# Optimization experiments

Hardware: AMD Instinct MI355X
Metric: run time of the kernel (lower is better)

## Reference

```python
import jax, jax.numpy as jnp
import numpy as np

N_NODES = 50000


def gcn_conv(x, W, b, src, dst, n_nodes):
    """PyG-style GCNConv: add self-loops, symmetric norm, transform-then-aggregate."""
    E = src.shape[0]
    loop = jnp.arange(n_nodes, dtype=src.dtype)
    src_sl = jnp.concatenate([src, loop])  # [E + N]
    dst_sl = jnp.concatenate([dst, loop])
    # degree (incl. self loops) at destination nodes, unit edge weights
    deg = jax.ops.segment_sum(jnp.ones(E + n_nodes, dtype=x.dtype), dst_sl,
                              num_segments=n_nodes)
    deg_inv_sqrt = jnp.where(deg > 0, jax.lax.rsqrt(deg), 0.0)
    norm = deg_inv_sqrt[src_sl] * deg_inv_sqrt[dst_sl]  # [E + N]
    h = x @ W  # [N, out] transform first (cheaper than transforming messages)
    msg = h[src_sl] * norm[:, None]  # gather + scale, [E+N, out]
    out = jax.ops.segment_sum(msg, dst_sl, num_segments=n_nodes)  # scatter-add
    return out + b


def setup_inputs() -> dict:
    key = jax.random.key(0)
    k = jax.random.split(key, 8)
    in_f, hid = 128, 128
    E, EL = 800000, 200000
    x = jax.random.normal(k[0], (N_NODES, in_f), dtype=jnp.float32)
    edge_index = jax.random.randint(k[1], (2, E), 0, N_NODES, dtype=jnp.int64)
    edge_label_index = jax.random.randint(k[2], (2, EL), 0, N_NODES, dtype=jnp.int64)
    s1 = 1.0 / np.sqrt(in_f)
    s2 = 1.0 / np.sqrt(hid)
    W1 = jax.random.uniform(k[3], (in_f, hid), jnp.float32, -s1, s1)
    b1 = jnp.zeros((hid,), jnp.float32)
    W2 = jax.random.uniform(k[4], (hid, hid), jnp.float32, -s2, s2)
    b2 = jnp.zeros((hid,), jnp.float32)
    return {"x": x, "edge_index": edge_index, "edge_label_index": edge_label_index,
            "W1": W1, "b1": b1, "W2": W2, "b2": b2}


def reference(x, edge_index, edge_label_index, W1, b1, W2, b2):
    src, dst = edge_index[0], edge_index[1]
    z = gcn_conv(x, W1, b1, src, dst, N_NODES)
    z = jax.nn.relu(z)
    z = gcn_conv(z, W2, b2, src, dst, N_NODES)
    ls, ld = edge_label_index[0], edge_label_index[1]
    prob = jnp.sum(z[ls] * z[ld], axis=1)  # gather-dot decode, [E_label]
    return jax.nn.sigmoid(prob)
```

## Files before the change

### kernel.cpp

```cpp
#include <hip/hip_runtime.h>
#include <hip/hip_fp16.h>
#include <math.h>

#define NN 50000
#define F 128
#define NB 512

typedef _Float16 half8 __attribute__((ext_vector_type(8)));
typedef float floatx4 __attribute__((ext_vector_type(4)));
typedef unsigned int uintx4 __attribute__((ext_vector_type(4)));

__global__ __launch_bounds__(256) void hist_kernel(const int* __restrict__ dst,
                                                   int* __restrict__ blockhist, int E) {
    __shared__ int h[256];
    int t = threadIdx.x;
    h[t] = 0;
    __syncthreads();
    int chunk = (E + NB - 1) / NB;
    int s = blockIdx.x * chunk;
    int e = min(E, s + chunk);
    for (int i = s + t; i < e; i += 256) atomicAdd(&h[dst[i] >> 8], 1);
    __syncthreads();
    blockhist[blockIdx.x * 256 + t] = h[t];
}

__global__ __launch_bounds__(256) void scanA_kernel(int* __restrict__ blockhist,
                                                    int* __restrict__ btot) {
    __shared__ int wsum[4];
    int b = blockIdx.x;
    int t = threadIdx.x;
    int lane = t & 63, wv = t >> 6;
    int v0 = blockhist[t * 256 + b];
    int v1 = blockhist[(t + 256) * 256 + b];

    int inc = v0;
#pragma unroll
    for (int o = 1; o < 64; o <<= 1) {
        int u = __shfl_up(inc, o, 64);
        if (lane >= o) inc += u;
    }
    if (lane == 63) wsum[wv] = inc;
    __syncthreads();
    int woff = 0, tot0 = 0;
#pragma unroll
    for (int w2 = 0; w2 < 4; ++w2) {
        if (w2 < wv) woff += wsum[w2];
        tot0 += wsum[w2];
    }
    int p0 = woff + inc - v0;
    __syncthreads();

    int inc1 = v1;
#pragma unroll
    for (int o = 1; o < 64; o <<= 1) {
        int u = __shfl_up(inc1, o, 64);
        if (lane >= o) inc1 += u;
    }
    if (lane == 63) wsum[wv] = inc1;
    __syncthreads();
    int woff1 = 0, tot1 = 0;
#pragma unroll
    for (int w2 = 0; w2 < 4; ++w2) {
        if (w2 < wv) woff1 += wsum[w2];
        tot1 += wsum[w2];
    }
    int p1 = tot0 + woff1 + inc1 - v1;

    blockhist[t * 256 + b] = p0;
    blockhist[(t + 256) * 256 + b] = p1;
    if (t == 255) btot[b] = tot0 + tot1;
}

__global__ __launch_bounds__(256) void part_kernel(const int* __restrict__ src,
                                                   const int* __restrict__ dst,
                                                   const int* __restrict__ blockhist,
                                                   const int* __restrict__ btot,
                                                   unsigned int* __restrict__ part, int E) {
    __shared__ int cur[256];
    __shared__ int wsum[4];
    int t = threadIdx.x;
    int lane = t & 63, wv = t >> 6;
    int bt = btot[t];
    int inc = bt;
#pragma unroll
    for (int o = 1; o < 64; o <<= 1) {
        int u = __shfl_up(inc, o, 64);
        if (lane >= o) inc += u;
    }
    if (lane == 63) wsum[wv] = inc;
    __syncthreads();
    int woff = 0;
#pragma unroll
    for (int w2 = 0; w2 < 4; ++w2)
        if (w2 < wv) woff += wsum[w2];
    int bs = woff + inc - bt;
    cur[t] = blockhist[blockIdx.x * 256 + t] + bs;
    __syncthreads();

    int chunk = (E + NB - 1) / NB;
    int s = blockIdx.x * chunk;
    int e = min(E, s + chunk);
    for (int i = s + t; i < e; i += 256) {
        int dd = dst[i];
        int p = atomicAdd(&cur[dd >> 8], 1);
        part[p] = ((unsigned int)(dd & 255) << 16) | (unsigned int)src[i];
    }
}

__global__ __launch_bounds__(256) void bucket_kernel(
    const unsigned int* __restrict__ part, const int* __restrict__ btot,
    int* __restrict__ rowptr, float* __restrict__ dinv,
    unsigned short* __restrict__ csr, int n, int E, int nbuck) {
    __shared__ int cnt[256];
    __shared__ int wtot[4];
    __shared__ unsigned int stage[8192];
    __shared__ int sS, sM;
    int b = blockIdx.x;
    int t = threadIdx.x;
    int lane = t & 63, wv = t >> 6;

    int bt = btot[t];
    int inc = bt;
#pragma unroll
    for (int o = 1; o < 64; o <<= 1) {
        int u = __shfl_up(inc, o, 64);
        if (lane >= o) inc += u;
    }
    if (lane == 63) wtot[wv] = inc;
    __syncthreads();
    int woff = 0;
#pragma unroll
    for (int w2 = 0; w2 < 4; ++w2)
        if (w2 < wv) woff += wtot[w2];
    int excl0 = woff + inc - bt;
    if (t == b) { sS = excl0; sM = bt; }
    cnt[t] = 0;
    __syncthreads();

    int s = sS;
    int m = sM;
    bool fits = (m <= 8192);
    for (int i = t; i < m; i += 256) {
        unsigned int v = part[s + i];
        if (fits) stage[i] = v;
        atomicAdd(&cnt[(v >> 16) & 255], 1);
    }
    __syncthreads();
    int c = cnt[t];
    int inc2 = c;
#pragma unroll
    for (int o = 1; o < 64; o <<= 1) {
        int u = __shfl_up(inc2, o, 64);
        if (lane >= o) inc2 += u;
    }
    if (lane == 63) wtot[wv] = inc2;
    __syncthreads();
    int wo = 0;
#pragma unroll
    for (int w2 = 0; w2 < 4; ++w2)
        if (w2 < wv) wo += wtot[w2];
    int excl = wo + inc2 - c;
    int d = (b << 8) + t;
    if (d < n) {
        rowptr[d] = s + excl;
        dinv[d] = rsqrtf((float)(c + 1));
    }
    if (b == nbuck - 1 && t == 255) rowptr[n] = E;
    __syncthreads();
    cnt[t] = excl;
    __syncthreads();
    if (fits) {
        for (int i = t; i < m; i += 256) {
            unsigned int v = stage[i];
            int p = atomicAdd(&cnt[(v >> 16) & 255], 1);
            csr[s + p] = (unsigned short)(v & 0xFFFFu);
        }
    } else {
        for (int i = t; i < m; i += 256) {
            unsigned int v = part[s + i];
            int p = atomicAdd(&cnt[(v >> 16) & 255], 1);
            csr[s + p] = (unsigned short)(v & 0xFFFFu);
        }
    }
}

template <bool IN_F32>
__global__ __launch_bounds__(256) void gemm_kernel(
    const void* __restrict__ xin, const float* __restrict__ W,
    const float* __restrict__ dinv, __half* __restrict__ g, int n) {
    __shared__ union {
        unsigned short wt[F * F];
        float cs[64 * 132];
    } sm;
    int t = threadIdx.x;

#pragma unroll
    for (int i = 0; i < 16; ++i) {
        int f = (i * 256 + t) * 4;
        int k = f >> 7;
        int nn = f & 127;
        float4 w4 = *(const float4*)&W[f];
        sm.wt[(nn + 0) * F + (k ^ (((nn + 0) & 7) << 3))] = __half_as_ushort(__float2half_rn(w4.x));
        sm.wt[(nn + 1) * F + (k ^ (((nn + 1) & 7) << 3))] = __half_as_ushort(__float2half_rn(w4.y));
        sm.wt[(nn + 2) * F + (k ^ (((nn + 2) & 7) << 3))] = __half_as_ushort(__float2half_rn(w4.z));
        sm.wt[(nn + 3) * F + (k ^ (((nn + 3) & 7) << 3))] = __half_as_ushort(__float2half_rn(w4.w));
    }
    __syncthreads();

    int lane = t & 63;
    int wave = t >> 6;
    int r0 = blockIdx.x * 64;
    int arow = min(r0 + wave * 16 + (lane & 15), n - 1);
    int klane = (lane >> 4) * 8;

    union FU { uintx4 u; half8 h; };
    FU af[4];
    if (IN_F32) {
        const float* xp = (const float*)xin + (size_t)arow * F + klane;
#pragma unroll
        for (int ks = 0; ks < 4; ++ks) {
            float4 a = *(const float4*)(xp + ks * 32);
            float4 b = *(const float4*)(xp + ks * 32 + 4);
            af[ks].h[0] = (_Float16)a.x; af[ks].h[1] = (_Float16)a.y;
            af[ks].h[2] = (_Float16)a.z; af[ks].h[3] = (_Float16)a.w;
            af[ks].h[4] = (_Float16)b.x; af[ks].h[5] = (_Float16)b.y;
            af[ks].h[6] = (_Float16)b.z; af[ks].h[7] = (_Float16)b.w;
        }
    } else {
        const unsigned short* xp = (const unsigned short*)xin + (size_t)arow * F + klane;
#pragma unroll
        for (int ks = 0; ks < 4; ++ks) af[ks].u = *(const uintx4*)(xp + ks * 32);
    }

    int swz = (lane & 7) << 3;
    int colb = (lane & 15) * F;

    floatx4 acc[8];
#pragma unroll
    for (int nt = 0; nt < 8; ++nt) acc[nt] = (floatx4)(0.0f);

#pragma unroll
    for (int ks = 0; ks < 4; ++ks) {
        int k0 = ks * 32 + klane;
        int ko = k0 ^ swz;
#pragma unroll
        for (int nt = 0; nt < 8; ++nt) {
            FU bf;
            bf.u = *(const uintx4*)&sm.wt[nt * 16 * F + colb + ko];
            acc[nt] = __builtin_amdgcn_mfma_f32_16x16x32_f16(af[ks].h, bf.h, acc[nt], 0, 0, 0);
        }
    }

    __syncthreads();
    int crow = wave * 16 + (lane >> 4) * 4;
#pragma unroll
    for (int nt = 0; nt < 8; ++nt) {
        int ccol = nt * 16 + (lane & 15);
#pragma unroll
        for (int r = 0; r < 4; ++r) sm.cs[(crow + r) * 132 + ccol] = acc[nt][r];
    }
    __syncthreads();

#pragma unroll
    for (int i = 0; i < 16; ++i) {
        int f = i * 256 + t;
        int row = f >> 6;
        int cp = f & 63;
        int grow = r0 + row;
        if (grow < n) {
            float lo = sm.cs[row * 132 + cp * 2];
            float hi = sm.cs[row * 132 + cp * 2 + 1];
            float di = dinv[grow];
            ((__half2*)g)[(size_t)grow * 64 + cp] = __floats2half2_rn(lo * di, hi * di);
        }
    }
}

template <bool RELU, bool OUT_HALF>
__global__ __launch_bounds__(256) void aggregate_kernel(
    const int* __restrict__ rowptr, const unsigned short* __restrict__ csr_src,
    const float* __restrict__ dinv, const __half* __restrict__ g,
    const float* __restrict__ bias, void* __restrict__ out, int n) {
    int lane = threadIdx.x & 63;
    int d = (blockIdx.x * blockDim.x + threadIdx.x) >> 6;
    if (d >= n) return;

    const __half2* gp = (const __half2*)g;

    float2 f = __half22float2(gp[(size_t)d * 64 + lane]);
    float accx = f.x, accy = f.y;

    int e = rowptr[d];
    int end = rowptr[d + 1];
    for (; e + 16 <= end; e += 16) {
        __half2 v[16];
#pragma unroll
        for (int j = 0; j < 16; ++j) {
            int s = csr_src[e + j];
            v[j] = gp[(size_t)s * 64 + lane];
        }
#pragma unroll
        for (int j = 0; j < 16; ++j) {
            float2 fv = __half22float2(v[j]);
            accx += fv.x;
            accy += fv.y;
        }
    }
    for (; e + 4 <= end; e += 4) {
        __half2 v[4];
#pragma unroll
        for (int j = 0; j < 4; ++j) {
            int s = csr_src[e + j];
            v[j] = gp[(size_t)s * 64 + lane];
        }
#pragma unroll
        for (int j = 0; j < 4; ++j) {
            float2 fv = __half22float2(v[j]);
            accx += fv.x;
            accy += fv.y;
        }
    }
    for (; e < end; ++e) {
        int s = csr_src[e];
        float2 fv = __half22float2(gp[(size_t)s * 64 + lane]);
        accx += fv.x;
        accy += fv.y;
    }

    float di = dinv[d];
    int c = lane * 2;
    float2 b = *(const float2*)&bias[c];
    float rx = di * accx + b.x;
    float ry = di * accy + b.y;
    if (RELU) {
        rx = fmaxf(rx, 0.0f);
        ry = fmaxf(ry, 0.0f);
    }
    if (OUT_HALF) {
        ((__half2*)out)[(size_t)d * 64 + lane] = __floats2half2_rn(rx, ry);
    } else {
        float2 r = {rx, ry};
        *(float2*)&((float*)out)[(size_t)d * F + c] = r;
    }
}

__global__ __launch_bounds__(256) void decode_kernel(
    const int* __restrict__ ls, const int* __restrict__ ld,
    const __half* __restrict__ z, float* __restrict__ out, int EL) {
    int t = threadIdx.x;
    int lane = t & 63;
    int grp = lane >> 4;
    int q = lane & 15;
    int wv = (blockIdx.x * blockDim.x + t) >> 6;
    int e = wv * 4 + grp;
    int ec = min(e, EL - 1);
    int a = ls[ec];
    int b = ld[ec];

    union FU { uintx4 u; __half2 h2[4]; };
    FU ua, ub;
    ua.u = *(const uintx4*)((const unsigned short*)z + (size_t)a * F + q * 8);
    ub.u = *(const uintx4*)((const unsigned short*)z + (size_t)b * F + q * 8);
    float s = 0.0f;
#pragma unroll
    for (int j = 0; j < 4; ++j) {
        float2 fa = __half22float2(ua.h2[j]);
        float2 fb = __half22float2(ub.h2[j]);
        s += fa.x * fb.x + fa.y * fb.y;
    }
#pragma unroll
    for (int off = 8; off; off >>= 1) s += __shfl_xor(s, off, 16);
    if (q == 0 && e < EL) out[e] = 1.0f / (1.0f + expf(-s));
}

extern "C" void kernel_launch(void* const* d_in, const int* in_sizes, int n_in,
                              void* d_out, int out_size, void* d_ws, size_t ws_size,
                              hipStream_t stream) {
    const float* x = (const float*)d_in[0];
    const int* ei = (const int*)d_in[1];
    const int* eli = (const int*)d_in[2];
    const float* W1 = (const float*)d_in[3];
    const float* b1 = (const float*)d_in[4];
    const float* W2 = (const float*)d_in[5];
    const float* b2 = (const float*)d_in[6];
    float* out = (float*)d_out;

    int E = in_sizes[1] / 2;
    int EL = in_sizes[2] / 2;
    const int* src = ei;
    const int* dst = ei + E;
    const int* ls = eli;
    const int* ld = eli + EL;
    int n = in_sizes[0] / F;
    int nbuck = (n + 255) >> 8;

    char* ws = (char*)d_ws;
    float*          dinv      = (float*)(ws);
    int*            rowptr    = (int*)(ws + (1u << 20));
    int*            blockhist = (int*)(ws + (2u << 20));
    int*            btot      = (int*)(ws + 2883584u);
    unsigned int*   part      = (unsigned int*)(ws + (3u << 20));
    unsigned short* csr       = (unsigned short*)(ws + 6815744u);
    __half*         gh        = (__half*)(ws + (22u << 20));
    __half*         z1h       = (__half*)(ws + (35u << 20));
    __half*         z2        = (__half*)(ws + (48u << 20));

    const int BS = 256;
    int gemm_blocks = (n + 63) / 64;
    int agg_blocks = (n + 3) / 4;
    int dec_blocks = (EL + 15) / 16;

    hist_kernel<<<NB, BS, 0, stream>>>(dst, blockhist, E);
    scanA_kernel<<<256, BS, 0, stream>>>(blockhist, btot);
    part_kernel<<<NB, BS, 0, stream>>>(src, dst, blockhist, btot, part, E);
    bucket_kernel<<<nbuck, BS, 0, stream>>>(part, btot, rowptr, dinv, csr, n, E, nbuck);

    gemm_kernel<true><<<gemm_blocks, BS, 0, stream>>>(x, W1, dinv, gh, n);
    aggregate_kernel<true, true><<<agg_blocks, BS, 0, stream>>>(rowptr, csr, dinv, gh, b1, z1h, n);

    gemm_kernel<false><<<gemm_blocks, BS, 0, stream>>>(z1h, W2, dinv, gh, n);
    aggregate_kernel<false, true><<<agg_blocks, BS, 0, stream>>>(rowptr, csr, dinv, gh, b2, z2, n);

    decode_kernel<<<dec_blocks, BS, 0, stream>>>(ls, ld, z2, out, EL);
}
```

Measured before the change: 170.4 us.

## Split aggregation by feature quarter with edge-parallel subgroups per wave

The aggregation kernel now gives each block one 32-feature quarter of the columns, ordered so that all blocks for a quarter run together. Each wave processes 8 destination nodes in turn, with four 16-lane subgroups striding over the edges and combining their sums by cross-lane shuffle. The aim is to shrink the gathered working set to a quarter of the feature matrix for better cache hit rates and to spread edge gathers across subgroups. In exchange, each node's indices and rowptr are read four times, gathers become 64-byte segments, and the per-node loop is serial without deep unrolling.

```diff
diff --git a/kernel.cpp b/kernel.cpp
--- a/kernel.cpp
+++ b/kernel.cpp
@@ -276,71 +276,55 @@
     }
 }
 
-template <bool RELU, bool OUT_HALF>
+template <bool RELU>
 __global__ __launch_bounds__(256) void aggregate_kernel(
     const int* __restrict__ rowptr, const unsigned short* __restrict__ csr_src,
     const float* __restrict__ dinv, const __half* __restrict__ g,
-    const float* __restrict__ bias, void* __restrict__ out, int n) {
-    int lane = threadIdx.x & 63;
-    int d = (blockIdx.x * blockDim.x + threadIdx.x) >> 6;
-    if (d >= n) return;
-
+    const float* __restrict__ bias, __half* __restrict__ out, int n, int nb_d) {
+    int t = threadIdx.x;
+    int lane = t & 63;
+    int wave = t >> 6;
+    int sg = lane >> 4;
+    int lq = lane & 15;
+    int qt = blockIdx.x / nb_d;
+    int bidx = blockIdx.x - qt * nb_d;
+    int qh = qt * 16 + lq;
     const __half2* gp = (const __half2*)g;
-
-    float2 f = __half22float2(gp[(size_t)d * 64 + lane]);
-    float accx = f.x, accy = f.y;
-
-    int e = rowptr[d];
-    int end = rowptr[d + 1];
-    for (; e + 16 <= end; e += 16) {
-        __half2 v[16];
-#pragma unroll
-        for (int j = 0; j < 16; ++j) {
-            int s = csr_src[e + j];
-            v[j] = gp[(size_t)s * 64 + lane];
-        }
-#pragma unroll
-        for (int j = 0; j < 16; ++j) {
-            float2 fv = __half22float2(v[j]);
+    __half2* op = (__half2*)out;
+    float2 bb = *(const float2*)&bias[qt * 32 + lq * 2];
+
+    int d0 = bidx * 32 + wave * 8;
+#pragma unroll 1
+    for (int i = 0; i < 8; ++i) {
+        int d = d0 + i;
+        if (d >= n) return;
+        int e = rowptr[d];
+        int end = rowptr[d + 1];
+        float accx = 0.0f, accy = 0.0f;
+        if (sg == 0) {
+            float2 f = __half22float2(gp[(size_t)d * 64 + qh]);
+            accx = f.x; accy = f.y;
+        }
+        for (int ee = e + sg; ee < end; ee += 4) {
+            int s = csr_src[ee];
+            float2 fv = __half22float2(gp[(size_t)s * 64 + qh]);
             accx += fv.x;
             accy += fv.y;
         }
-    }
-    for (; e + 4 <= end; e += 4) {
-        __half2 v[4];
-#pragma unroll
-        for (int j = 0; j < 4; ++j) {
-            int s = csr_src[e + j];
-            v[j] = gp[(size_t)s * 64 + lane];
-        }
-#pragma unroll
-        for (int j = 0; j < 4; ++j) {
-            float2 fv = __half22float2(v[j]);
-            accx += fv.x;
-            accy += fv.y;
-        }
-    }
-    for (; e < end; ++e) {
-        int s = csr_src[e];
-        float2 fv = __half22float2(gp[(size_t)s * 64 + lane]);
-        accx += fv.x;
-        accy += fv.y;
-    }
-
-    float di = dinv[d];
-    int c = lane * 2;
-    float2 b = *(const float2*)&bias[c];
-    float rx = di * accx + b.x;
-    float ry = di * accy + b.y;
-    if (RELU) {
-        rx = fmaxf(rx, 0.0f);
-        ry = fmaxf(ry, 0.0f);
-    }
-    if (OUT_HALF) {
-        ((__half2*)out)[(size_t)d * 64 + lane] = __floats2half2_rn(rx, ry);
-    } else {
-        float2 r = {rx, ry};
-        *(float2*)&((float*)out)[(size_t)d * F + c] = r;
+        accx += __shfl_xor(accx, 16, 64);
+        accy += __shfl_xor(accy, 16, 64);
+        accx += __shfl_xor(accx, 32, 64);
+        accy += __shfl_xor(accy, 32, 64);
+        if (sg == 0) {
+            float di = dinv[d];
+            float rx = di * accx + bb.x;
+            float ry = di * accy + bb.y;
+            if (RELU) {
+                rx = fmaxf(rx, 0.0f);
+                ry = fmaxf(ry, 0.0f);
+            }
+            op[(size_t)d * 64 + qh] = __floats2half2_rn(rx, ry);
+        }
     }
 }
 
@@ -407,7 +391,8 @@
 
     const int BS = 256;
     int gemm_blocks = (n + 63) / 64;
-    int agg_blocks = (n + 3) / 4;
+    int nb_d = (n + 31) / 32;
+    int agg_blocks = 4 * nb_d;
     int dec_blocks = (EL + 15) / 16;
 
     hist_kernel<<<NB, BS, 0, stream>>>(dst, blockhist, E);
@@ -416,10 +401,10 @@
     bucket_kernel<<<nbuck, BS, 0, stream>>>(part, btot, rowptr, dinv, csr, n, E, nbuck);
 
     gemm_kernel<true><<<gemm_blocks, BS, 0, stream>>>(x, W1, dinv, gh, n);
-    aggregate_kernel<true, true><<<agg_blocks, BS, 0, stream>>>(rowptr, csr, dinv, gh, b1, z1h, n);
+    aggregate_kernel<true><<<agg_blocks, BS, 0, stream>>>(rowptr, csr, dinv, gh, b1, z1h, n, nb_d);
 
     gemm_kernel<false><<<gemm_blocks, BS, 0, stream>>>(z1h, W2, dinv, gh, n);
-    aggregate_kernel<false, true><<<agg_blocks, BS, 0, stream>>>(rowptr, csr, dinv, gh, b2, z2, n);
+    aggregate_kernel<false><<<agg_blocks, BS, 0, stream>>>(rowptr, csr, dinv, gh, b2, z2, n, nb_d);
 
     decode_kernel<<<dec_blocks, BS, 0, stream>>>(ls, ld, z2, out, EL);
 }
```

New measurement: 315.9 us. 1.85x slower.
